# Kernel optimization log

Measured on AMD Instinct MI355X. Metric: run time of the kernel, lower is better.

## Reference

```python
import jax, jax.numpy as jnp
import numpy as np

EPS = 1e-05

def setup_inputs() -> dict:
    key = jax.random.key(0)
    k1, k2, k3 = jax.random.split(key, 3)
    B, S, D_IN, D_OUT = 4, 2048, 4096, 12288
    x = jax.random.normal(k1, (B, S, D_IN), dtype=jnp.float32)
    weight = jax.random.normal(k2, (D_OUT, D_IN), dtype=jnp.float32) * (1.0 / np.sqrt(D_IN))
    bias = jnp.zeros((D_OUT,), dtype=jnp.float32)
    ln_weight = jnp.ones((D_IN,), dtype=jnp.float32)
    ln_bias = jnp.zeros((D_IN,), dtype=jnp.float32)
    return {"x": x, "weight": weight, "bias": bias, "ln_weight": ln_weight, "ln_bias": ln_bias}

def reference(x, weight, bias, ln_weight, ln_bias):
    # LayerNorm over last dim
    mean = jnp.mean(x, axis=-1, keepdims=True)
    var = jnp.mean(jnp.square(x - mean), axis=-1, keepdims=True)
    normed = (x - mean) * jax.lax.rsqrt(var + EPS) * ln_weight + ln_bias
    # Linear: y = normed @ W^T + b
    return jnp.einsum('bsd,od->bso', normed, weight) + bias
```

## Files before the change

kernel.cpp:

```cpp
#include <hip/hip_runtime.h>
#include <hip/hip_bf16.h>
#include <stdint.h>

typedef __attribute__((ext_vector_type(8))) short short8_t;
typedef __attribute__((ext_vector_type(4))) float f32x4;

__device__ __forceinline__ unsigned short f2bf(float f) {
  union { float f; unsigned int u; } a;
  a.f = f;
  unsigned int u = a.u;
  u += 0x7fffu + ((u >> 16) & 1u);
  return (unsigned short)(u >> 16);
}

__device__ __forceinline__ void gload_lds16(const void* g, void* l) {
  __builtin_amdgcn_global_load_lds(
      (const __attribute__((address_space(1))) void*)g,
      (__attribute__((address_space(3))) void*)l, 16, 0, 0);
}

constexpr int D_IN = 4096;

__global__ __launch_bounds__(256) void ln_bf16_kernel(
    const float* __restrict__ x, const float* __restrict__ lnw,
    const float* __restrict__ lnb, unsigned short* __restrict__ out) {
  const int row = blockIdx.x;
  const int tid = threadIdx.x;
  const float* xr = x + (size_t)row * D_IN;

  f32x4 v[4];
  float sum = 0.f, sq = 0.f;
#pragma unroll
  for (int i = 0; i < 4; ++i) {
    v[i] = __builtin_nontemporal_load(
        reinterpret_cast<const f32x4*>(xr + i * 1024 + tid * 4));
    sum += v[i][0] + v[i][1] + v[i][2] + v[i][3];
    sq += v[i][0]*v[i][0] + v[i][1]*v[i][1] + v[i][2]*v[i][2] + v[i][3]*v[i][3];
  }
#pragma unroll
  for (int off = 32; off > 0; off >>= 1) {
    sum += __shfl_down(sum, off, 64);
    sq  += __shfl_down(sq, off, 64);
  }
  __shared__ float s_sum[4], s_sq[4];
  if ((tid & 63) == 0) { s_sum[tid >> 6] = sum; s_sq[tid >> 6] = sq; }
  __syncthreads();
  const float fs = s_sum[0] + s_sum[1] + s_sum[2] + s_sum[3];
  const float fq = s_sq[0] + s_sq[1] + s_sq[2] + s_sq[3];
  const float mean = fs * (1.f / D_IN);
  const float var = fq * (1.f / D_IN) - mean * mean;
  const float rstd = rsqrtf(var + 1e-5f);

  unsigned short* orow = out + (size_t)row * D_IN;
#pragma unroll
  for (int i = 0; i < 4; ++i) {
    const int col = i * 1024 + tid * 4;
    const f32x4 w = *reinterpret_cast<const f32x4*>(lnw + col);
    const f32x4 b = *reinterpret_cast<const f32x4*>(lnb + col);
    ushort4 o;
    o.x = f2bf((v[i][0] - mean) * rstd * w[0] + b[0]);
    o.y = f2bf((v[i][1] - mean) * rstd * w[1] + b[1]);
    o.z = f2bf((v[i][2] - mean) * rstd * w[2] + b[2]);
    o.w = f2bf((v[i][3] - mean) * rstd * w[3] + b[3]);
    *reinterpret_cast<ushort4*>(orow + col) = o;
  }
}

__global__ __launch_bounds__(256) void f32_to_bf16_kernel(
    const float* __restrict__ in, unsigned short* __restrict__ out) {
  const size_t i = ((size_t)blockIdx.x * 256 + threadIdx.x) * 8;
  const f32x4 a = __builtin_nontemporal_load(reinterpret_cast<const f32x4*>(in + i));
  const f32x4 b = __builtin_nontemporal_load(reinterpret_cast<const f32x4*>(in + i + 4));
  ushort4 lo, hi;
  lo.x = f2bf(a[0]); lo.y = f2bf(a[1]); lo.z = f2bf(a[2]); lo.w = f2bf(a[3]);
  hi.x = f2bf(b[0]); hi.y = f2bf(b[1]); hi.z = f2bf(b[2]); hi.w = f2bf(b[3]);
  *reinterpret_cast<ushort4*>(out + i) = lo;
  *reinterpret_cast<ushort4*>(out + i + 4) = hi;
}


#define RDA(S, KK, ROW) \
  (*reinterpret_cast<const short8_t*>(((KK) ? aB1 : aB0) + (S)*32768 + (ROW)*128))
#define RDB(S, KK, ROW) \
  (*reinterpret_cast<const short8_t*>(((KK) ? bB1 : bB0) + (S)*32768 + (ROW)*128))

#define READ_A(S, MH)                                          \
  _Pragma("unroll") for (int m_ = 0; m_ < 4; ++m_) {           \
    af[m_][0] = RDA(S, 0, (MH)*64 + m_*16);                    \
    af[m_][1] = RDA(S, 1, (MH)*64 + m_*16);                    \
  }

#define READ_B(S, NH)                                          \
  _Pragma("unroll") for (int n_ = 0; n_ < 2; ++n_) {           \
    bfr[(NH)*2+n_][0] = RDB(S, 0, ((NH)*2+n_)*16);             \
    bfr[(NH)*2+n_][1] = RDB(S, 1, ((NH)*2+n_)*16);             \
  }

#define MFMA_Q(MH, NH)                                                         \
  _Pragma("unroll") for (int kk_ = 0; kk_ < 2; ++kk_) {                        \
    _Pragma("unroll") for (int m_ = 0; m_ < 4; ++m_) {                         \
      _Pragma("unroll") for (int n_ = 0; n_ < 2; ++n_)                         \
        acc[(MH)*4+m_][(NH)*2+n_] = __builtin_amdgcn_mfma_f32_16x16x32_bf16(   \
            af[m_][kk_], bfr[(NH)*2+n_][kk_], acc[(MH)*4+m_][(NH)*2+n_], 0, 0, 0); \
    }                                                                          \
  }

#define STAGE_A(S, U, KT) \
  gload_lds16(aSrc + (size_t)((U)*64) * K + (size_t)(KT)*64, ldsAw + (S)*32768 + (U)*8192)
#define STAGE_B(S, U, KT) \
  gload_lds16(bSrc + (size_t)((U)*64) * K + (size_t)(KT)*64, ldsBw + (S)*32768 + (U)*8192)

#define PH_MID                                         \
  __builtin_amdgcn_s_barrier();                        \
  asm volatile("s_waitcnt lgkmcnt(0)" ::: "memory");   \
  __builtin_amdgcn_sched_barrier(0);                   \
  __builtin_amdgcn_s_setprio(1)
#define PH_END                                         \
  __builtin_amdgcn_sched_barrier(0);                   \
  __builtin_amdgcn_s_setprio(0);                       \
  __builtin_amdgcn_s_barrier();                        \
  asm volatile("" ::: "memory")
#define PH_END_V(N)                                    \
  __builtin_amdgcn_sched_barrier(0);                   \
  __builtin_amdgcn_s_setprio(0);                       \
  asm volatile("s_waitcnt vmcnt(" #N ")" ::: "memory");\
  __builtin_amdgcn_s_barrier();                        \
  asm volatile("" ::: "memory")

__global__ __launch_bounds__(512, 2) void gemm_8phase(
    const unsigned short* __restrict__ A,
    const unsigned short* __restrict__ B,
    const float* __restrict__ bias,
    float* __restrict__ C,
    int M, int N, int K, int NYB, int BXP) {
  extern __shared__ char smem[];
  const int tid = threadIdx.x;
  const int lane = tid & 63;
  const int wid = tid >> 6;
  const int wr = wid >> 2, wc = wid & 3;
  const int fr = lane & 15;
  const int q16 = (lane >> 4) * 16;
  const int wr128 = wr * 128;
  const int wc64 = wc * 64;

  const int id = blockIdx.x;
  const int xcd = id & 7;
  const int slot = id >> 3;
  const int by = slot % NYB;
  const int bx = xcd * BXP + slot / NYB;
  const int m0 = by * 256, n0 = bx * 256;

  const int s_log = (tid * 16) ^ (((tid >> 3) & 7) << 4);
  const int rsw = s_log >> 7;
  const int csw = (s_log & 127) >> 1;
  const unsigned short* aSrc = A + (size_t)(m0 + rsw) * K + csw;
  const unsigned short* bSrc = B + (size_t)(n0 + rsw) * K + csw;

  char* const ldsAw = smem + wid * 1024;
  char* const ldsBw = smem + 65536 + wid * 1024;

  const int s7 = (fr & 7) << 4;
  const char* const aB0 = smem + (wr128 + fr) * 128 + (q16 ^ s7);
  const char* const aB1 = smem + (wr128 + fr) * 128 + ((64 + q16) ^ s7);
  const char* const bB0 = smem + 65536 + (wc64 + fr) * 128 + (q16 ^ s7);
  const char* const bB1 = smem + 65536 + (wc64 + fr) * 128 + ((64 + q16) ^ s7);

  f32x4 acc[8][4] = {};
  short8_t af[4][2], bfr[4][2];

  STAGE_A(0,0,0); STAGE_A(0,1,0); STAGE_A(0,2,0); STAGE_A(0,3,0);
  STAGE_B(0,0,0); STAGE_B(0,1,0); STAGE_B(0,2,0); STAGE_B(0,3,0);
  STAGE_A(1,0,1); STAGE_A(1,1,1); STAGE_A(1,2,1); STAGE_A(1,3,1);
  STAGE_B(1,0,1); STAGE_B(1,1,1);
  asm volatile("s_waitcnt vmcnt(6)" ::: "memory");
  __builtin_amdgcn_s_barrier();
  asm volatile("" ::: "memory");

  const int NT = K >> 7;
  for (int t = 0; t < NT - 1; ++t) {
    const int k1 = 2*t + 1, k2 = 2*t + 2, k3 = 2*t + 3;
    READ_A(0, 0) READ_B(0, 0)
    STAGE_B(1,2,k1); STAGE_B(1,3,k1);
    asm volatile("s_waitcnt lgkmcnt(8)" ::: "memory");
    PH_MID; MFMA_Q(0,0) PH_END;
    READ_B(0, 1)
    STAGE_A(0,0,k2); STAGE_A(0,2,k2);
    PH_MID; MFMA_Q(0,1) PH_END;
    READ_A(0, 1)
    STAGE_B(0,0,k2); STAGE_B(0,1,k2);
    PH_MID; MFMA_Q(1,0) PH_END;
    STAGE_A(0,1,k2); STAGE_A(0,3,k2);
    PH_MID; MFMA_Q(1,1) PH_END_V(6);
    READ_A(1, 0) READ_B(1, 0)
    STAGE_B(0,2,k2); STAGE_B(0,3,k2);
    asm volatile("s_waitcnt lgkmcnt(8)" ::: "memory");
    PH_MID; MFMA_Q(0,0) PH_END;
    READ_B(1, 1)
    STAGE_A(1,0,k3); STAGE_A(1,2,k3);
    PH_MID; MFMA_Q(0,1) PH_END;
    READ_A(1, 1)
    STAGE_B(1,0,k3); STAGE_B(1,1,k3);
    PH_MID; MFMA_Q(1,0) PH_END;
    STAGE_A(1,1,k3); STAGE_A(1,3,k3);
    PH_MID; MFMA_Q(1,1) PH_END_V(6);
  }
  {
    const int k1 = 2*NT - 1;
    READ_A(0, 0) READ_B(0, 0)
    STAGE_B(1,2,k1); STAGE_B(1,3,k1);
    PH_MID; MFMA_Q(0,0) PH_END;
    READ_B(0, 1)
    PH_MID; MFMA_Q(0,1) PH_END;
    READ_A(0, 1)
    PH_MID; MFMA_Q(1,0) PH_END;
    PH_MID; MFMA_Q(1,1) PH_END_V(0);
    READ_A(1, 0) READ_B(1, 0)
    PH_MID; MFMA_Q(0,0) PH_END;
    READ_B(1, 1)
    PH_MID; MFMA_Q(0,1) PH_END;
    READ_A(1, 1)
    PH_MID; MFMA_Q(1,0) PH_END;
    PH_MID; MFMA_Q(1,1)
    __builtin_amdgcn_sched_barrier(0);
    __builtin_amdgcn_s_setprio(0);
  }

  __syncthreads();
  float* const buf0 = (float*)smem;
  float* const buf1 = (float*)smem + 64 * 260;
  const int cr = (lane >> 4) * 4;
  float bv[4];
#pragma unroll
  for (int ni = 0; ni < 4; ++ni) bv[ni] = bias[n0 + wc64 + ni * 16 + fr];

#pragma unroll
  for (int half = 0; half < 2; ++half) {
    float* const wbuf = (wr == 0) ? buf0 : buf1;
#pragma unroll
    for (int mi4 = 0; mi4 < 4; ++mi4) {
      const int mi = half * 4 + mi4;
#pragma unroll
      for (int j = 0; j < 4; ++j) {
        const int lr = mi4 * 16 + cr + j;
#pragma unroll
        for (int ni = 0; ni < 4; ++ni)
          wbuf[lr * 260 + wc64 + ni * 16 + fr] = acc[mi][ni][j] + bv[ni];
      }
    }
    __syncthreads();
#pragma unroll
    for (int i = 0; i < 16; ++i) {
      const int idx = wid * 16 + i;
      const float* src = (idx < 64 ? buf0 + idx * 260 : buf1 + (idx - 64) * 260) + lane * 4;
      const int grow = m0 + (idx < 64 ? half * 64 + idx : 128 + half * 64 + (idx - 64));
      const f32x4 vv = *reinterpret_cast<const f32x4*>(src);
      __builtin_nontemporal_store(
          vv, reinterpret_cast<f32x4*>(C + (size_t)grow * N + n0) + lane);
    }
    __syncthreads();
  }
}

extern "C" void kernel_launch(void* const* d_in, const int* in_sizes, int n_in,
                              void* d_out, int out_size, void* d_ws, size_t ws_size,
                              hipStream_t stream) {
  const float* x    = (const float*)d_in[0];
  const float* w    = (const float*)d_in[1];
  const float* bias = (const float*)d_in[2];
  const float* lnw  = (const float*)d_in[3];
  const float* lnb  = (const float*)d_in[4];
  float* out = (float*)d_out;

  const int DIN  = 4096;
  const int M    = in_sizes[0] / DIN;
  const int DOUT = in_sizes[2];

  unsigned short* normA = (unsigned short*)d_ws;
  unsigned short* wB    = normA + (size_t)M * DIN;

  ln_bf16_kernel<<<M, 256, 0, stream>>>(x, lnw, lnb, normA);
  f32_to_bf16_kernel<<<((size_t)DOUT * DIN) / (256 * 8), 256, 0, stream>>>(w, wB);

  const int nwg = (M / 256) * (DOUT / 256);
  const int smem_bytes = 2 * 64 * 260 * 4 > 131072 ? 2 * 64 * 260 * 4 : 131072;
  (void)hipFuncSetAttribute((const void*)gemm_8phase,
                            hipFuncAttributeMaxDynamicSharedMemorySize, 163840);
  gemm_8phase<<<nwg, 512, smem_bytes, stream>>>(normA, wB, bias, out,
                                                M, DOUT, DIN, M / 256, (DOUT / 256) / 8);
}
```

Before: 777.5 us.

## Switch GEMM inner loop to 32x32x16 bf16 MFMA tiles

Replaces the 16x16x32 MFMA fragments with 32x32x16 MFMA instructions. This changes the per-wave LDS fragment addressing (swizzled pointers per k-fragment), the accumulator layout (f32x16) and the epilogue row mapping. The larger MFMA tile needs fewer LDS reads per flop and fewer instructions per phase. It also moves the lgkmcnt wait from before the MFMAs to the end of each phase and drops the sched_barriers, which gives the compiler more freedom to interleave reads with MFMAs but risks waiting on LDS data inside the compute phase.

```diff
diff --git a/kernel.cpp b/kernel.cpp
--- a/kernel.cpp
+++ b/kernel.cpp
@@ -4,6 +4,7 @@
 
 typedef __attribute__((ext_vector_type(8))) short short8_t;
 typedef __attribute__((ext_vector_type(4))) float f32x4;
+typedef __attribute__((ext_vector_type(16))) float f32x16;
 
 __device__ __forceinline__ unsigned short f2bf(float f) {
   union { float f; unsigned int u; } a;
@@ -79,30 +80,25 @@
 }
 
 
-#define RDA(S, KK, ROW) \
-  (*reinterpret_cast<const short8_t*>(((KK) ? aB1 : aB0) + (S)*32768 + (ROW)*128))
-#define RDB(S, KK, ROW) \
-  (*reinterpret_cast<const short8_t*>(((KK) ? bB1 : bB0) + (S)*32768 + (ROW)*128))
-
-#define READ_A(S, MH)                                          \
-  _Pragma("unroll") for (int m_ = 0; m_ < 4; ++m_) {           \
-    af[m_][0] = RDA(S, 0, (MH)*64 + m_*16);                    \
-    af[m_][1] = RDA(S, 1, (MH)*64 + m_*16);                    \
-  }
-
-#define READ_B(S, NH)                                          \
-  _Pragma("unroll") for (int n_ = 0; n_ < 2; ++n_) {           \
-    bfr[(NH)*2+n_][0] = RDB(S, 0, ((NH)*2+n_)*16);             \
-    bfr[(NH)*2+n_][1] = RDB(S, 1, ((NH)*2+n_)*16);             \
-  }
-
-#define MFMA_Q(MH, NH)                                                         \
-  _Pragma("unroll") for (int kk_ = 0; kk_ < 2; ++kk_) {                        \
-    _Pragma("unroll") for (int m_ = 0; m_ < 4; ++m_) {                         \
-      _Pragma("unroll") for (int n_ = 0; n_ < 2; ++n_)                         \
-        acc[(MH)*4+m_][(NH)*2+n_] = __builtin_amdgcn_mfma_f32_16x16x32_bf16(   \
-            af[m_][kk_], bfr[(NH)*2+n_][kk_], acc[(MH)*4+m_][(NH)*2+n_], 0, 0, 0); \
-    }                                                                          \
+#define RDF(P, IMM) (*reinterpret_cast<const short8_t*>((P) + (IMM)))
+
+#define READ_A(S, MH)                                                 \
+  _Pragma("unroll") for (int i_ = 0; i_ < 2; ++i_) {                  \
+    _Pragma("unroll") for (int kf_ = 0; kf_ < 4; ++kf_)               \
+      af[i_][kf_] = RDF(aA[kf_], (S)*32768 + ((MH)*2 + i_)*4096);     \
+  }
+#define READ_B0(S)                                                    \
+  _Pragma("unroll") for (int kf_ = 0; kf_ < 4; ++kf_)                 \
+      bf0[kf_] = RDF(bA[kf_], (S)*32768);
+#define READ_B1(S)                                                    \
+  _Pragma("unroll") for (int kf_ = 0; kf_ < 4; ++kf_)                 \
+      bf1[kf_] = RDF(bA[kf_], (S)*32768 + 4096);
+
+#define MFMA_Q(MH, NH, BF)                                            \
+  _Pragma("unroll") for (int kf_ = 0; kf_ < 4; ++kf_) {               \
+    _Pragma("unroll") for (int i_ = 0; i_ < 2; ++i_)                  \
+      acc[(MH)*2 + i_][NH] = __builtin_amdgcn_mfma_f32_32x32x16_bf16( \
+          af[i_][kf_], BF[kf_], acc[(MH)*2 + i_][NH], 0, 0, 0);       \
   }
 
 #define STAGE_A(S, U, KT) \
@@ -112,18 +108,15 @@
 
 #define PH_MID                                         \
   __builtin_amdgcn_s_barrier();                        \
-  asm volatile("s_waitcnt lgkmcnt(0)" ::: "memory");   \
-  __builtin_amdgcn_sched_barrier(0);                   \
   __builtin_amdgcn_s_setprio(1)
 #define PH_END                                         \
-  __builtin_amdgcn_sched_barrier(0);                   \
   __builtin_amdgcn_s_setprio(0);                       \
+  asm volatile("s_waitcnt lgkmcnt(0)" ::: "memory");   \
   __builtin_amdgcn_s_barrier();                        \
   asm volatile("" ::: "memory")
 #define PH_END_V(N)                                    \
-  __builtin_amdgcn_sched_barrier(0);                   \
   __builtin_amdgcn_s_setprio(0);                       \
-  asm volatile("s_waitcnt vmcnt(" #N ")" ::: "memory");\
+  asm volatile("s_waitcnt lgkmcnt(0)\n\ts_waitcnt vmcnt(" #N ")" ::: "memory");\
   __builtin_amdgcn_s_barrier();                        \
   asm volatile("" ::: "memory")
 
@@ -138,8 +131,9 @@
   const int lane = tid & 63;
   const int wid = tid >> 6;
   const int wr = wid >> 2, wc = wid & 3;
-  const int fr = lane & 15;
-  const int q16 = (lane >> 4) * 16;
+  const int l31 = lane & 31;
+  const int kh = lane >> 5;
+  const int l7 = lane & 7;
   const int wr128 = wr * 128;
   const int wc64 = wc * 64;
 
@@ -159,14 +153,17 @@
   char* const ldsAw = smem + wid * 1024;
   char* const ldsBw = smem + 65536 + wid * 1024;
 
-  const int s7 = (fr & 7) << 4;
-  const char* const aB0 = smem + (wr128 + fr) * 128 + (q16 ^ s7);
-  const char* const aB1 = smem + (wr128 + fr) * 128 + ((64 + q16) ^ s7);
-  const char* const bB0 = smem + 65536 + (wc64 + fr) * 128 + (q16 ^ s7);
-  const char* const bB1 = smem + 65536 + (wc64 + fr) * 128 + ((64 + q16) ^ s7);
-
-  f32x4 acc[8][4] = {};
-  short8_t af[4][2], bfr[4][2];
+  const char* aA[4];
+  const char* bA[4];
+#pragma unroll
+  for (int kf = 0; kf < 4; ++kf) {
+    const int sl = ((((kf << 1) | kh) ^ l7) << 4);
+    aA[kf] = smem + (wr128 + l31) * 128 + sl;
+    bA[kf] = smem + 65536 + (wc64 + l31) * 128 + sl;
+  }
+
+  f32x16 acc[4][2] = {};
+  short8_t af[2][4], bf0[4], bf1[4];
 
   STAGE_A(0,0,0); STAGE_A(0,1,0); STAGE_A(0,2,0); STAGE_A(0,3,0);
   STAGE_B(0,0,0); STAGE_B(0,1,0); STAGE_B(0,2,0); STAGE_B(0,3,0);
@@ -179,72 +176,67 @@
   const int NT = K >> 7;
   for (int t = 0; t < NT - 1; ++t) {
     const int k1 = 2*t + 1, k2 = 2*t + 2, k3 = 2*t + 3;
-    READ_A(0, 0) READ_B(0, 0)
+    READ_A(0, 0) READ_B0(0)
     STAGE_B(1,2,k1); STAGE_B(1,3,k1);
-    asm volatile("s_waitcnt lgkmcnt(8)" ::: "memory");
-    PH_MID; MFMA_Q(0,0) PH_END;
-    READ_B(0, 1)
+    PH_MID; MFMA_Q(0,0,bf0) PH_END;
+    READ_B1(0)
     STAGE_A(0,0,k2); STAGE_A(0,2,k2);
-    PH_MID; MFMA_Q(0,1) PH_END;
+    PH_MID; MFMA_Q(0,1,bf1) PH_END;
     READ_A(0, 1)
     STAGE_B(0,0,k2); STAGE_B(0,1,k2);
-    PH_MID; MFMA_Q(1,0) PH_END;
+    PH_MID; MFMA_Q(1,0,bf0) PH_END;
     STAGE_A(0,1,k2); STAGE_A(0,3,k2);
-    PH_MID; MFMA_Q(1,1) PH_END_V(6);
-    READ_A(1, 0) READ_B(1, 0)
+    PH_MID; MFMA_Q(1,1,bf1) PH_END_V(6);
+    READ_A(1, 0) READ_B0(1)
     STAGE_B(0,2,k2); STAGE_B(0,3,k2);
-    asm volatile("s_waitcnt lgkmcnt(8)" ::: "memory");
-    PH_MID; MFMA_Q(0,0) PH_END;
-    READ_B(1, 1)
+    PH_MID; MFMA_Q(0,0,bf0) PH_END;
+    READ_B1(1)
     STAGE_A(1,0,k3); STAGE_A(1,2,k3);
-    PH_MID; MFMA_Q(0,1) PH_END;
+    PH_MID; MFMA_Q(0,1,bf1) PH_END;
     READ_A(1, 1)
     STAGE_B(1,0,k3); STAGE_B(1,1,k3);
-    PH_MID; MFMA_Q(1,0) PH_END;
+    PH_MID; MFMA_Q(1,0,bf0) PH_END;
     STAGE_A(1,1,k3); STAGE_A(1,3,k3);
-    PH_MID; MFMA_Q(1,1) PH_END_V(6);
+    PH_MID; MFMA_Q(1,1,bf1) PH_END_V(6);
   }
   {
     const int k1 = 2*NT - 1;
-    READ_A(0, 0) READ_B(0, 0)
+    READ_A(0, 0) READ_B0(0)
     STAGE_B(1,2,k1); STAGE_B(1,3,k1);
-    PH_MID; MFMA_Q(0,0) PH_END;
-    READ_B(0, 1)
-    PH_MID; MFMA_Q(0,1) PH_END;
+    PH_MID; MFMA_Q(0,0,bf0) PH_END;
+    READ_B1(0)
+    PH_MID; MFMA_Q(0,1,bf1) PH_END;
     READ_A(0, 1)
-    PH_MID; MFMA_Q(1,0) PH_END;
-    PH_MID; MFMA_Q(1,1) PH_END_V(0);
-    READ_A(1, 0) READ_B(1, 0)
-    PH_MID; MFMA_Q(0,0) PH_END;
-    READ_B(1, 1)
-    PH_MID; MFMA_Q(0,1) PH_END;
+    PH_MID; MFMA_Q(1,0,bf0) PH_END;
+    PH_MID; MFMA_Q(1,1,bf1) PH_END_V(0);
+    READ_A(1, 0) READ_B0(1)
+    PH_MID; MFMA_Q(0,0,bf0) PH_END;
+    READ_B1(1)
+    PH_MID; MFMA_Q(0,1,bf1) PH_END;
     READ_A(1, 1)
-    PH_MID; MFMA_Q(1,0) PH_END;
-    PH_MID; MFMA_Q(1,1)
-    __builtin_amdgcn_sched_barrier(0);
+    PH_MID; MFMA_Q(1,0,bf0) PH_END;
+    PH_MID; MFMA_Q(1,1,bf1)
     __builtin_amdgcn_s_setprio(0);
   }
 
   __syncthreads();
   float* const buf0 = (float*)smem;
   float* const buf1 = (float*)smem + 64 * 260;
-  const int cr = (lane >> 4) * 4;
-  float bv[4];
-#pragma unroll
-  for (int ni = 0; ni < 4; ++ni) bv[ni] = bias[n0 + wc64 + ni * 16 + fr];
+  float bv[2];
+#pragma unroll
+  for (int nt = 0; nt < 2; ++nt) bv[nt] = bias[n0 + wc64 + nt * 32 + l31];
 
 #pragma unroll
   for (int half = 0; half < 2; ++half) {
     float* const wbuf = (wr == 0) ? buf0 : buf1;
 #pragma unroll
-    for (int mi4 = 0; mi4 < 4; ++mi4) {
-      const int mi = half * 4 + mi4;
-#pragma unroll
-      for (int j = 0; j < 4; ++j) {
-        const int lr = mi4 * 16 + cr + j;
-#pragma unroll
-        for (int ni = 0; ni < 4; ++ni)
-          wbuf[lr * 260 + wc64 + ni * 16 + fr] = acc[mi][ni][j] + bv[ni];
+    for (int im = 0; im < 2; ++im) {
+#pragma unroll
+      for (int reg = 0; reg < 16; ++reg) {
+        const int lr = im * 32 + (reg & 3) + 8 * (reg >> 2) + 4 * kh;
+#pragma unroll
+        for (int nt = 0; nt < 2; ++nt)
+          wbuf[lr * 260 + wc64 + nt * 32 + l31] = acc[half*2 + im][nt][reg] + bv[nt];
       }
     }
     __syncthreads();
```

New measurement: 879.2 us. +13.1%, slower.
